# Optimization experiments

Hardware: AMD Instinct MI355X
Metric: run time of the kernel (lower is better)

## Reference

```python
import jax, jax.numpy as jnp
import numpy as np

B, DM, H, M, K = 2, 256, 4, 4096, 16
DIM = DM // H  # per-head feature dim = 64


def _proj(x, W, b):
    # 1x1 Conv2d on channels-first (B, C, M, K): pointwise linear over channels
    return jnp.einsum('oi,bimk->bomk', W, x) + b[None, :, None, None]


def setup_inputs() -> dict:
    rng = jax.random.key(0)
    ks = jax.random.split(rng, 11)
    s = 1.0 / np.sqrt(DM)
    return {
        'query': jax.random.normal(ks[0], (B, DM, M, 1), jnp.float32),
        'key':   jax.random.normal(ks[1], (B, DM, M, K), jnp.float32),
        'value': jax.random.normal(ks[2], (B, DM, M, K), jnp.float32),
        'Wq': jax.random.normal(ks[3], (DM, DM), jnp.float32) * s,
        'bq': jax.random.normal(ks[4], (DM,), jnp.float32) * 0.01,
        'Wk': jax.random.normal(ks[5], (DM, DM), jnp.float32) * s,
        'bk': jax.random.normal(ks[6], (DM,), jnp.float32) * 0.01,
        'Wv': jax.random.normal(ks[7], (DM, DM), jnp.float32) * s,
        'bv': jax.random.normal(ks[8], (DM,), jnp.float32) * 0.01,
        'Wm': jax.random.normal(ks[9], (DM, DM), jnp.float32) * s,
        'bm': jax.random.normal(ks[10], (DM,), jnp.float32) * 0.01,
    }


def reference(query, key, value, Wq, bq, Wk, bk, Wv, bv, Wm, bm):
    # project; torch view(B, dim, heads, -1) on channels-first => channel c -> (d=c//H, h=c%H)
    q = _proj(query, Wq, bq).reshape(B, DIM, H, M)          # (b, d, h, m)
    k = _proj(key,   Wk, bk).reshape(B, DIM, H, M, K)        # (b, d, h, m, k)
    v = _proj(value, Wv, bv).reshape(B, DIM, H, M, K)
    scores = jnp.einsum('bfhm,bfhmk->bhmk', q, k) / np.sqrt(DIM).astype(np.float32)
    prob = jax.nn.softmax(scores, axis=-1)                   # softmax over kn neighbors
    x = jnp.einsum('bhmk,bdhmk->bdhm', prob, v)              # (b, d, h, m)
    out = _proj(x.reshape(B, DM, M, 1), Wm, bm)              # merge 1x1 conv
    prob_sum = jnp.sum(prob, axis=1)                         # (b, m, k)
    return out, prob_sum
```

## Files before the change

### kernel.cpp

```cpp
#include <hip/hip_runtime.h>
#include <stdint.h>

#define DM_ 256
#define H_ 4
#define M_ 4096
#define KN_ 16
#define B_ 2
#define MK_ (M_*KN_)

typedef __attribute__((ext_vector_type(8))) short short8;
typedef __attribute__((ext_vector_type(4))) float f32x4;
typedef __attribute__((ext_vector_type(4))) unsigned short u16x4;

static __device__ __forceinline__ unsigned short f2bf(float x) {
  union { float f; uint32_t u; } v; v.f = x;
  uint32_t u = v.u + (0x7FFFu + ((v.u >> 16) & 1u));
  return (unsigned short)(u >> 16);
}
static __device__ __forceinline__ float u2f(uint32_t u) {
  union { uint32_t u; float f; } v; v.u = u; return v.f;
}

static __device__ __forceinline__ int swz512(int col, int kbyte) {
  int f = ((col >> 2) & 7) ^ ((col & 1) << 2);
  return (col << 9) + (kbyte ^ (f << 4));
}

__global__ void prep2(const float* __restrict__ Wq, const float* __restrict__ bq,
                      const float* __restrict__ Wk, const float* __restrict__ Wv,
                      const float* __restrict__ bv, const float* __restrict__ Wm,
                      const float* __restrict__ bm,
                      unsigned short* __restrict__ W2T, unsigned short* __restrict__ Wmv,
                      float* __restrict__ qb2, float* __restrict__ btot) {
  int t = blockIdx.x * 512 + threadIdx.x;
  if (t < 262144) {
    int j = t & 7, lane = (t >> 3) & 63, rowblk = (t >> 9) & 63, kstep = t >> 15;
    int row = rowblk * 16 + (lane & 15);
    int k = kstep * 32 + (lane >> 4) * 8 + j;
    int h = row >> 8, c = row & 255;
    float v = 0.f;
#pragma unroll 8
    for (int d = 0; d < 64; ++d) v += Wq[(4 * d + h) * 256 + k] * Wk[(4 * d + h) * 256 + c];
    W2T[t] = f2bf(v);
  } else if (t < 524288) {
    int e = t - 262144;
    int j = e & 7, lane = (e >> 3) & 63, rowblk = (e >> 9) & 15, kstep = e >> 13;
    int o = rowblk * 16 + (lane & 15);
    int kidx = kstep * 32 + (lane >> 4) * 8 + j;
    int c = kidx >> 2, h = kidx & 3;
    float v = 0.f;
#pragma unroll 8
    for (int d = 0; d < 64; ++d) v += Wm[o * 256 + 4 * d + h] * Wv[(4 * d + h) * 256 + c];
    Wmv[e] = f2bf(v);
  } else if (t < 525312) {
    int r = t - 524288; int h = r >> 8, c = r & 255;
    float v = 0.f;
#pragma unroll 8
    for (int d = 0; d < 64; ++d) v += bq[4 * d + h] * Wk[(4 * d + h) * 256 + c];
    qb2[r] = v;
  } else if (t < 525568) {
    int o = t - 525312;
    float v = bm[o];
#pragma unroll 8
    for (int c2 = 0; c2 < 256; ++c2) v += Wm[o * 256 + c2] * bv[c2];
    btot[o] = v;
  }
}

__global__ __launch_bounds__(512)
void qw_gemm(const float* __restrict__ query, const unsigned short* __restrict__ W2T,
             const float* __restrict__ qb2, unsigned short* __restrict__ qWbuf) {
  __shared__ unsigned short Xl[32 * 256];
  const int tid = threadIdx.x;
  const int lane = tid & 63, wid = tid >> 6;
  const int wr = wid >> 1, wc = wid & 1;
  const int mt = blockIdx.x & 127;
  const int rt = (blockIdx.x >> 7) & 3;
  const int b = blockIdx.x >> 9;
  const int m0 = mt * 32;
  const float* Xb = query + (size_t)b * DM_ * M_ + m0;
  const int c4 = 4 * (tid & 7);
  const int ch0 = 4 * (tid >> 3);
  float4 f[4];
#pragma unroll
  for (int i = 0; i < 4; ++i) f[i] = *(const float4*)(Xb + (size_t)(ch0 + i) * M_ + c4);
#pragma unroll
  for (int j = 0; j < 4; ++j) {
    u16x4 u = { f2bf(((const float*)&f[0])[j]), f2bf(((const float*)&f[1])[j]),
                f2bf(((const float*)&f[2])[j]), f2bf(((const float*)&f[3])[j]) };
    *(u16x4*)((char*)Xl + swz512(c4 + j, 2 * ch0)) = u;
  }
  __syncthreads();
  f32x4 acc[4] = {};
  const int bcol = wc * 16 + (lane & 15);
  const int rdk = 16 * (lane >> 4);
  short8 a_cur[4], a_nxt[4];
#pragma unroll
  for (int fi = 0; fi < 4; ++fi)
    a_cur[fi] = *(const short8*)(W2T + (size_t)(((rt * 16 + wr * 4 + fi) * 64 + lane) * 8));
#pragma unroll
  for (int kgs = 0; kgs < 8; ++kgs) {
    if (kgs < 7) {
#pragma unroll
      for (int fi = 0; fi < 4; ++fi)
        a_nxt[fi] = *(const short8*)(W2T + (size_t)((((kgs + 1) * 64 + rt * 16 + wr * 4 + fi) * 64 + lane) * 8));
    }
    short8 bb = *(const short8*)((const char*)Xl + swz512(bcol, 64 * kgs + rdk));
#pragma unroll
    for (int fi = 0; fi < 4; ++fi)
      acc[fi] = __builtin_amdgcn_mfma_f32_16x16x32_bf16(a_cur[fi], bb, acc[fi], 0, 0, 0);
#pragma unroll
    for (int fi = 0; fi < 4; ++fi) a_cur[fi] = a_nxt[fi];
  }
#pragma unroll
  for (int fi = 0; fi < 4; ++fi) {
#pragma unroll
    for (int r = 0; r < 4; ++r) {
      const int rr = rt * 256 + wr * 64 + fi * 16 + (lane >> 4) * 4 + r;
      qWbuf[(size_t)(b * 1024 + rr) * M_ + m0 + bcol] = f2bf(acc[fi][r] + qb2[rr]);
    }
  }
}

__global__ __launch_bounds__(1024, 8)
void fused_attn(const float* __restrict__ key, const float* __restrict__ value,
                const unsigned short* __restrict__ qW, const unsigned short* __restrict__ Wmv,
                const float* __restrict__ btot, float* __restrict__ out,
                float* __restrict__ psum) {
  __shared__ unsigned short sh[16384];
  const int tid = threadIdx.x;
  const int lane = tid & 63;
  const int vb = (blockIdx.x & 7) * 64 + (blockIdx.x >> 3);
  const int b = vb >> 8;
  const int m0 = (vb & 255) * 16;
  {
    const int c = tid & 255, h = tid >> 8;
    const unsigned short* src = qW + ((size_t)(b * 1024 + h * 256 + c)) * M_ + m0;
    uint4 rv[2];
    rv[0] = *(const uint4*)(src);
    rv[1] = *(const uint4*)(src + 8);
    const unsigned short* rs = (const unsigned short*)rv;
#pragma unroll
    for (int q = 0; q < 16; ++q) {
      const int slot = (q + c) & 15;
      sh[c * 64 + slot * 4 + h] = rs[q];
    }
  }
  __syncthreads();
  const int mq = tid >> 6;
  const int cs = (tid >> 2) & 15;
  const int kq = tid & 3;
  const float* kp = key + (size_t)(b * 256) * 65536 + (size_t)m0 * 16;
  const float* vp = value + (size_t)(b * 256) * 65536 + (size_t)m0 * 16;
  const int moff = mq * 16 + kq * 4;
  f32x4 ps0 = {}, ps1 = {}, ps2 = {}, ps3 = {};
#pragma unroll 4
  for (int i = 0; i < 16; ++i) {
    const int c = i * 16 + cs;
    const f32x4 kv = *(const f32x4*)(kp + (size_t)c * 65536 + moff);
    const int slot = (mq + c) & 15;
    const uint2 qv = *(const uint2*)&sh[c * 64 + slot * 4];
    ps0 += kv * u2f(qv.x << 16);
    ps1 += kv * u2f(qv.x & 0xffff0000u);
    ps2 += kv * u2f(qv.y << 16);
    ps3 += kv * u2f(qv.y & 0xffff0000u);
  }
#pragma unroll
  for (int j = 0; j < 4; ++j) {
    ps0[j] += __shfl_xor(ps0[j], 4); ps0[j] += __shfl_xor(ps0[j], 8);
    ps0[j] += __shfl_xor(ps0[j], 16); ps0[j] += __shfl_xor(ps0[j], 32);
    ps1[j] += __shfl_xor(ps1[j], 4); ps1[j] += __shfl_xor(ps1[j], 8);
    ps1[j] += __shfl_xor(ps1[j], 16); ps1[j] += __shfl_xor(ps1[j], 32);
    ps2[j] += __shfl_xor(ps2[j], 4); ps2[j] += __shfl_xor(ps2[j], 8);
    ps2[j] += __shfl_xor(ps2[j], 16); ps2[j] += __shfl_xor(ps2[j], 32);
    ps3[j] += __shfl_xor(ps3[j], 4); ps3[j] += __shfl_xor(ps3[j], 8);
    ps3[j] += __shfl_xor(ps3[j], 16); ps3[j] += __shfl_xor(ps3[j], 32);
  }
  f32x4 pr0, pr1, pr2, pr3;
#define SOFT(ps, pr) { \
    f32x4 s = ps * 0.125f; \
    float mx = fmaxf(fmaxf(s[0], s[1]), fmaxf(s[2], s[3])); \
    mx = fmaxf(mx, __shfl_xor(mx, 1)); mx = fmaxf(mx, __shfl_xor(mx, 2)); \
    f32x4 e; \
    e[0] = __expf(s[0] - mx); e[1] = __expf(s[1] - mx); \
    e[2] = __expf(s[2] - mx); e[3] = __expf(s[3] - mx); \
    float sm = e[0] + e[1] + e[2] + e[3]; \
    sm += __shfl_xor(sm, 1); sm += __shfl_xor(sm, 2); \
    const float inv = 1.f / sm; \
    pr[0] = e[0] * inv; pr[1] = e[1] * inv; pr[2] = e[2] * inv; pr[3] = e[3] * inv; \
  }
  SOFT(ps0, pr0) SOFT(ps1, pr1) SOFT(ps2, pr2) SOFT(ps3, pr3)
#undef SOFT
  if (cs == 0) {
    f32x4 pp = pr0 + pr1 + pr2 + pr3;
    *(f32x4*)(psum + ((size_t)b * M_ + m0 + mq) * KN_ + kq * 4) = pp;
  }
  __syncthreads();
#pragma unroll 4
  for (int i = 0; i < 16; ++i) {
    const int c = i * 16 + cs;
    const f32x4 vv = *(const f32x4*)(vp + (size_t)c * 65536 + moff);
    float p0 = vv[0] * pr0[0] + vv[1] * pr0[1] + vv[2] * pr0[2] + vv[3] * pr0[3];
    float p1 = vv[0] * pr1[0] + vv[1] * pr1[1] + vv[2] * pr1[2] + vv[3] * pr1[3];
    float p2 = vv[0] * pr2[0] + vv[1] * pr2[1] + vv[2] * pr2[2] + vv[3] * pr2[3];
    float p3 = vv[0] * pr3[0] + vv[1] * pr3[1] + vv[2] * pr3[2] + vv[3] * pr3[3];
    p0 += __shfl_xor(p0, 1); p0 += __shfl_xor(p0, 2);
    p1 += __shfl_xor(p1, 1); p1 += __shfl_xor(p1, 2);
    p2 += __shfl_xor(p2, 1); p2 += __shfl_xor(p2, 2);
    p3 += __shfl_xor(p3, 1); p3 += __shfl_xor(p3, 2);
    if (kq == 0) {
      uint2 o;
      o.x = (uint32_t)f2bf(p0) | ((uint32_t)f2bf(p1) << 16);
      o.y = (uint32_t)f2bf(p2) | ((uint32_t)f2bf(p3) << 16);
      *(uint2*)((char*)sh + ((mq * 2048 + c * 8) ^ ((mq & 7) << 4))) = o;
    }
  }
  __syncthreads();
  {
    const int wid = tid >> 6;
    const int bcol = lane & 15;
    const int kgrp = lane >> 4;
    f32x4 acc = {};
    for (int kgs = 0; kgs < 32; ++kgs) {
      const int byte = (bcol * 2048 + kgs * 64 + kgrp * 16) ^ ((bcol & 7) << 4);
      const short8 bb = *(const short8*)((const char*)sh + byte);
      const short8 a0 = *(const short8*)(Wmv + (size_t)(((kgs * 16 + wid) * 64 + lane) * 8));
      acc = __builtin_amdgcn_mfma_f32_16x16x32_bf16(a0, bb, acc, 0, 0, 0);
    }
#pragma unroll
    for (int r = 0; r < 4; ++r) {
      const int o = wid * 16 + kgrp * 4 + r;
      out[((size_t)(b * DM_ + o)) * M_ + m0 + bcol] = acc[r] + btot[o];
    }
  }
}

extern "C" void kernel_launch(void* const* d_in, const int* in_sizes, int n_in,
                              void* d_out, int out_size, void* d_ws, size_t ws_size,
                              hipStream_t stream) {
  const float* query = (const float*)d_in[0];
  const float* key   = (const float*)d_in[1];
  const float* value = (const float*)d_in[2];
  const float* Wq = (const float*)d_in[3];
  const float* bq = (const float*)d_in[4];
  const float* Wk = (const float*)d_in[5];
  const float* bk = (const float*)d_in[6];  (void)bk;
  const float* Wv = (const float*)d_in[7];
  const float* bv = (const float*)d_in[8];
  const float* Wm = (const float*)d_in[9];
  const float* bm = (const float*)d_in[10];
  float* out  = (float*)d_out;
  float* psum = out + (size_t)B_ * DM_ * M_;

  const size_t Wmv_off  = 524288;
  const size_t qb2_off  = 1048576;
  const size_t btot_off = 1052672;
  const size_t qW_off   = 1053696;

  unsigned short* W2T   = (unsigned short*)d_ws;
  unsigned short* Wmv   = (unsigned short*)((char*)d_ws + Wmv_off);
  float* qb2            = (float*)((char*)d_ws + qb2_off);
  float* btot           = (float*)((char*)d_ws + btot_off);
  unsigned short* qWbuf = (unsigned short*)((char*)d_ws + qW_off);

  prep2<<<dim3(1027), dim3(512), 0, stream>>>(Wq, bq, Wk, Wv, bv, Wm, bm, W2T, Wmv, qb2, btot);
  qw_gemm<<<dim3(B_ * 4 * 128), dim3(512), 0, stream>>>(query, W2T, qb2, qWbuf);
  fused_attn<<<dim3(512), dim3(1024), 0, stream>>>(key, value, qWbuf, Wmv, btot, out, psum);
}
```

Before: 104.9 us.

## Remap thread work so each wave reads contiguous key/value rows, reduce via LDS

Each wave now handles one channel slice while its 64 lanes cover the 16 positions × 4 k-quads contiguously. Each global load of key/value therefore covers a contiguous 1 KB span instead of scattered 64-byte pieces. The cross-channel score reduction moves from wave shuffles to an LDS partial-sum buffer, padded against bank conflicts. A separate pass then computes the softmax and the prob_sum, and stores the probabilities in LDS for the value pass. This adds two barriers, extra LDS traffic, and a larger shared-memory footprint that could reduce occupancy.

```diff
diff --git a/kernel.cpp b/kernel.cpp
--- a/kernel.cpp
+++ b/kernel.cpp
@@ -127,9 +127,12 @@
                 const unsigned short* __restrict__ qW, const unsigned short* __restrict__ Wmv,
                 const float* __restrict__ btot, float* __restrict__ out,
                 float* __restrict__ psum) {
-  __shared__ unsigned short sh[16384];
+  __shared__ float ldsA[16 * 64 * 17];
+  __shared__ float ldsP[16 * 4 * 16];
+  unsigned short* qsl = (unsigned short*)ldsA;
   const int tid = threadIdx.x;
   const int lane = tid & 63;
+  const int w = tid >> 6;
   const int vb = (blockIdx.x & 7) * 64 + (blockIdx.x >> 3);
   const int b = vb >> 8;
   const int m0 = (vb & 255) * 16;
@@ -143,76 +146,85 @@
 #pragma unroll
     for (int q = 0; q < 16; ++q) {
       const int slot = (q + c) & 15;
-      sh[c * 64 + slot * 4 + h] = rs[q];
-    }
-  }
-  __syncthreads();
-  const int mq = tid >> 6;
-  const int cs = (tid >> 2) & 15;
-  const int kq = tid & 3;
-  const float* kp = key + (size_t)(b * 256) * 65536 + (size_t)m0 * 16;
-  const float* vp = value + (size_t)(b * 256) * 65536 + (size_t)m0 * 16;
-  const int moff = mq * 16 + kq * 4;
+      qsl[c * 64 + slot * 4 + h] = rs[q];
+    }
+  }
+  __syncthreads();
+  const int mp = lane >> 2;
+  const int kkq = lane & 3;
+  const size_t cbase = (size_t)(b * 256) * 65536 + (size_t)m0 * 16 + lane * 4;
   f32x4 ps0 = {}, ps1 = {}, ps2 = {}, ps3 = {};
 #pragma unroll 4
   for (int i = 0; i < 16; ++i) {
-    const int c = i * 16 + cs;
-    const f32x4 kv = *(const f32x4*)(kp + (size_t)c * 65536 + moff);
-    const int slot = (mq + c) & 15;
-    const uint2 qv = *(const uint2*)&sh[c * 64 + slot * 4];
+    const int c = i * 16 + w;
+    const f32x4 kv = *(const f32x4*)(key + cbase + (size_t)c * 65536);
+    const int slot = (mp + c) & 15;
+    const uint2 qv = *(const uint2*)&qsl[c * 64 + slot * 4];
     ps0 += kv * u2f(qv.x << 16);
     ps1 += kv * u2f(qv.x & 0xffff0000u);
     ps2 += kv * u2f(qv.y << 16);
     ps3 += kv * u2f(qv.y & 0xffff0000u);
   }
-#pragma unroll
-  for (int j = 0; j < 4; ++j) {
-    ps0[j] += __shfl_xor(ps0[j], 4); ps0[j] += __shfl_xor(ps0[j], 8);
-    ps0[j] += __shfl_xor(ps0[j], 16); ps0[j] += __shfl_xor(ps0[j], 32);
-    ps1[j] += __shfl_xor(ps1[j], 4); ps1[j] += __shfl_xor(ps1[j], 8);
-    ps1[j] += __shfl_xor(ps1[j], 16); ps1[j] += __shfl_xor(ps1[j], 32);
-    ps2[j] += __shfl_xor(ps2[j], 4); ps2[j] += __shfl_xor(ps2[j], 8);
-    ps2[j] += __shfl_xor(ps2[j], 16); ps2[j] += __shfl_xor(ps2[j], 32);
-    ps3[j] += __shfl_xor(ps3[j], 4); ps3[j] += __shfl_xor(ps3[j], 8);
-    ps3[j] += __shfl_xor(ps3[j], 16); ps3[j] += __shfl_xor(ps3[j], 32);
-  }
-  f32x4 pr0, pr1, pr2, pr3;
-#define SOFT(ps, pr) { \
-    f32x4 s = ps * 0.125f; \
-    float mx = fmaxf(fmaxf(s[0], s[1]), fmaxf(s[2], s[3])); \
-    mx = fmaxf(mx, __shfl_xor(mx, 1)); mx = fmaxf(mx, __shfl_xor(mx, 2)); \
-    f32x4 e; \
-    e[0] = __expf(s[0] - mx); e[1] = __expf(s[1] - mx); \
-    e[2] = __expf(s[2] - mx); e[3] = __expf(s[3] - mx); \
-    float sm = e[0] + e[1] + e[2] + e[3]; \
-    sm += __shfl_xor(sm, 1); sm += __shfl_xor(sm, 2); \
-    const float inv = 1.f / sm; \
-    pr[0] = e[0] * inv; pr[1] = e[1] * inv; pr[2] = e[2] * inv; pr[3] = e[3] * inv; \
-  }
-  SOFT(ps0, pr0) SOFT(ps1, pr1) SOFT(ps2, pr2) SOFT(ps3, pr3)
-#undef SOFT
-  if (cs == 0) {
-    f32x4 pp = pr0 + pr1 + pr2 + pr3;
-    *(f32x4*)(psum + ((size_t)b * M_ + m0 + mq) * KN_ + kq * 4) = pp;
-  }
-  __syncthreads();
+  __syncthreads();
+  {
+    float* scx = ldsA + w * 1088 + lane * 17;
+#pragma unroll
+    for (int j = 0; j < 4; ++j) {
+      scx[j]      = ps0[j];
+      scx[4 + j]  = ps1[j];
+      scx[8 + j]  = ps2[j];
+      scx[12 + j] = ps3[j];
+    }
+  }
+  __syncthreads();
+  {
+    const int mp2 = tid >> 6;
+    const int h2 = (lane >> 4) & 3;
+    const int kk = lane & 15;
+    const int lanep = mp2 * 4 + (kk >> 2);
+    const int idx = h2 * 4 + (kk & 3);
+    float sc = 0.f;
+#pragma unroll
+    for (int w2 = 0; w2 < 16; ++w2) sc += ldsA[w2 * 1088 + lanep * 17 + idx];
+    sc *= 0.125f;
+    float mx = sc;
+    mx = fmaxf(mx, __shfl_xor(mx, 1)); mx = fmaxf(mx, __shfl_xor(mx, 2));
+    mx = fmaxf(mx, __shfl_xor(mx, 4)); mx = fmaxf(mx, __shfl_xor(mx, 8));
+    const float e = __expf(sc - mx);
+    float sm = e;
+    sm += __shfl_xor(sm, 1); sm += __shfl_xor(sm, 2);
+    sm += __shfl_xor(sm, 4); sm += __shfl_xor(sm, 8);
+    const float pb = e / sm;
+    ldsP[(mp2 * 4 + h2) * 16 + kk] = pb;
+    float tot = pb;
+    tot += __shfl_xor(tot, 16); tot += __shfl_xor(tot, 32);
+    if (lane < 16)
+      psum[((size_t)b * M_ + m0 + mp2) * KN_ + kk] = tot;
+  }
+  __syncthreads();
+  {
+    const f32x4 pr0 = *(const f32x4*)&ldsP[(mp * 4 + 0) * 16 + kkq * 4];
+    const f32x4 pr1 = *(const f32x4*)&ldsP[(mp * 4 + 1) * 16 + kkq * 4];
+    const f32x4 pr2 = *(const f32x4*)&ldsP[(mp * 4 + 2) * 16 + kkq * 4];
+    const f32x4 pr3 = *(const f32x4*)&ldsP[(mp * 4 + 3) * 16 + kkq * 4];
 #pragma unroll 4
-  for (int i = 0; i < 16; ++i) {
-    const int c = i * 16 + cs;
-    const f32x4 vv = *(const f32x4*)(vp + (size_t)c * 65536 + moff);
-    float p0 = vv[0] * pr0[0] + vv[1] * pr0[1] + vv[2] * pr0[2] + vv[3] * pr0[3];
-    float p1 = vv[0] * pr1[0] + vv[1] * pr1[1] + vv[2] * pr1[2] + vv[3] * pr1[3];
-    float p2 = vv[0] * pr2[0] + vv[1] * pr2[1] + vv[2] * pr2[2] + vv[3] * pr2[3];
-    float p3 = vv[0] * pr3[0] + vv[1] * pr3[1] + vv[2] * pr3[2] + vv[3] * pr3[3];
-    p0 += __shfl_xor(p0, 1); p0 += __shfl_xor(p0, 2);
-    p1 += __shfl_xor(p1, 1); p1 += __shfl_xor(p1, 2);
-    p2 += __shfl_xor(p2, 1); p2 += __shfl_xor(p2, 2);
-    p3 += __shfl_xor(p3, 1); p3 += __shfl_xor(p3, 2);
-    if (kq == 0) {
-      uint2 o;
-      o.x = (uint32_t)f2bf(p0) | ((uint32_t)f2bf(p1) << 16);
-      o.y = (uint32_t)f2bf(p2) | ((uint32_t)f2bf(p3) << 16);
-      *(uint2*)((char*)sh + ((mq * 2048 + c * 8) ^ ((mq & 7) << 4))) = o;
+    for (int i = 0; i < 16; ++i) {
+      const int c = i * 16 + w;
+      const f32x4 vv = *(const f32x4*)(value + cbase + (size_t)c * 65536);
+      float p0 = pr0[0] * vv[0] + pr0[1] * vv[1] + pr0[2] * vv[2] + pr0[3] * vv[3];
+      float p1 = pr1[0] * vv[0] + pr1[1] * vv[1] + pr1[2] * vv[2] + pr1[3] * vv[3];
+      float p2 = pr2[0] * vv[0] + pr2[1] * vv[1] + pr2[2] * vv[2] + pr2[3] * vv[3];
+      float p3 = pr3[0] * vv[0] + pr3[1] * vv[1] + pr3[2] * vv[2] + pr3[3] * vv[3];
+      p0 += __shfl_xor(p0, 1); p0 += __shfl_xor(p0, 2);
+      p1 += __shfl_xor(p1, 1); p1 += __shfl_xor(p1, 2);
+      p2 += __shfl_xor(p2, 1); p2 += __shfl_xor(p2, 2);
+      p3 += __shfl_xor(p3, 1); p3 += __shfl_xor(p3, 2);
+      if (kkq == 0) {
+        uint2 o;
+        o.x = (uint32_t)f2bf(p0) | ((uint32_t)f2bf(p1) << 16);
+        o.y = (uint32_t)f2bf(p2) | ((uint32_t)f2bf(p3) << 16);
+        *(uint2*)((char*)ldsA + ((mp * 2048 + c * 8) ^ ((mp & 7) << 4))) = o;
+      }
     }
   }
   __syncthreads();
@@ -223,7 +235,7 @@
     f32x4 acc = {};
     for (int kgs = 0; kgs < 32; ++kgs) {
       const int byte = (bcol * 2048 + kgs * 64 + kgrp * 16) ^ ((bcol & 7) << 4);
-      const short8 bb = *(const short8*)((const char*)sh + byte);
+      const short8 bb = *(const short8*)((const char*)ldsA + byte);
       const short8 a0 = *(const short8*)(Wmv + (size_t)(((kgs * 16 + wid) * 64 + lane) * 8));
       acc = __builtin_amdgcn_mfma_f32_16x16x32_bf16(a0, bb, acc, 0, 0, 0);
     }
```

Result: no change. 103.3 us (-1.5%).
